# Kernel tuning notes

Measured on AMD Instinct MI355X. Metric: run time of the kernel, lower is better.

The kernel has to match this reference:

```python
import jax, jax.numpy as jnp
import numpy as np

LN_EPS = 1e-5


def setup_inputs() -> dict:
    key = jax.random.key(0)
    k1, k2 = jax.random.split(key, 2)
    B, C, D, H, W = 2, 96, 32, 128, 128
    out_dim = 2 * C
    x = jax.random.normal(k1, (B, C, D, H, W), dtype=jnp.float32)
    # nn.Linear(8*C, out_dim, bias=False): weight shape (out_dim, 8*C)
    w = jax.random.normal(k2, (out_dim, 8 * C), dtype=jnp.float32) * 0.02
    gamma = jnp.ones((8 * C,), dtype=jnp.float32)
    beta = jnp.zeros((8 * C,), dtype=jnp.float32)
    return {"x": x, "w": w, "gamma": gamma, "beta": beta}


def reference(x, w, gamma, beta):
    B, C, D, H, W = x.shape
    D2, H2, W2 = D // 2, H // 2, W // 2
    # Strided 2x2x2 gather: reshape then move (dd,hh,ww) offsets next to C.
    # torch.cat order [x0..x7] = (dd,hh,ww) lexicographic, dd most significant,
    # with C channels per block -> layout (..., dd, hh, ww, C) flattened.
    xr = x.reshape(B, C, D2, 2, H2, 2, W2, 2)
    xr = xr.transpose(0, 2, 4, 6, 3, 5, 7, 1)  # (B, D2, H2, W2, dd, hh, ww, C)
    xf = xr.reshape(B, D2, H2, W2, 8 * C)
    # LayerNorm over last dim
    mu = jnp.mean(xf, axis=-1, keepdims=True)
    xc = xf - mu
    var = jnp.mean(xc * xc, axis=-1, keepdims=True)
    xn = xc * jax.lax.rsqrt(var + LN_EPS) * gamma + beta
    # Linear (no bias): y = xn @ w.T
    y = jnp.einsum('bdhwc,oc->bdhwo', xn, w)
    # back to channels-first (B, out_dim, D2, H2, W2)
    return y.transpose(0, 4, 1, 2, 3)
```

## Files before the change

kernel.cpp:

```cpp
#include <hip/hip_runtime.h>
#include <hip/hip_bf16.h>

typedef __attribute__((ext_vector_type(8))) short short8;
typedef __attribute__((ext_vector_type(4))) float f32x4;

#define LN_EPS 1e-5f

__device__ __forceinline__ unsigned short f2bf(float f) {
  union { float f; unsigned u; } v; v.f = f;
  unsigned r = v.u + 0x7FFFu + ((v.u >> 16) & 1u);
  return (unsigned short)(r >> 16);
}

__device__ __forceinline__ int a_addr(int row, int colb) {
  return row * 1536 + (colb ^ ((row & 7) << 4));
}


__global__ __launch_bounds__(256) void pm_prep(
    const float* __restrict__ w, const float* __restrict__ g,
    const float* __restrict__ be, unsigned short* __restrict__ wg,
    float* __restrict__ sb) {
  const int o = blockIdx.x;
  const int t = threadIdx.x;
  __shared__ float red[256][2];
  float sa = 0.f, ba = 0.f;
#pragma unroll
  for (int u = 0; u < 3; ++u) {
    int kp = t + 256 * u;
    int dh = kp / 192;
    int rem = kp - dh * 192;
    int c = rem >> 1, ww = rem & 1;
    int k = dh * 192 + ww * 96 + c;
    float wv = w[o * 768 + k];
    float v = wv * g[k];
    sa += v;
    ba += wv * be[k];
    int NT = o >> 4, ks = kp >> 5, qq = (kp >> 3) & 3, jj = kp & 7;
    wg[(((NT * 24 + ks) * 64) + qq * 16 + (o & 15)) * 8 + jj] = f2bf(v);
  }
  red[t][0] = sa; red[t][1] = ba;
  __syncthreads();
  for (int s = 128; s > 0; s >>= 1) {
    if (t < s) { red[t][0] += red[t + s][0]; red[t][1] += red[t + s][1]; }
    __syncthreads();
  }
  if (t == 0) { sb[o] = red[0][0]; sb[192 + o] = red[0][1]; }
}

__global__ __launch_bounds__(256, 3) void pm_main(
    const float* __restrict__ x, const unsigned short* __restrict__ wg,
    const float* __restrict__ sb, float* __restrict__ out) {
  const int bid = blockIdx.x;
  const int wh = bid & 1;
  const int h2 = (bid >> 1) & 63;
  const int d2 = (bid >> 7) & 15;
  const int b = bid >> 11;
  const int t = threadIdx.x;
  const int lane = t & 63, wv = t >> 6;
  const int q = lane & 15, sc = lane >> 4;

  __shared__ __align__(16) unsigned char A_lds[32 * 1536];
  __shared__ float part[4][32][2];
  __shared__ float stats[32][2];

  const float* xb = x + (size_t)b * (96 * 32 * 128 * 128);
  const int cp0 = wv * 12 + sc * 3;
  const float* pc[3];
#pragma unroll
  for (int i = 0; i < 3; ++i)
    pc[i] = xb + (size_t)(2 * (cp0 + i)) * 524288 + wh * 64 + 4 * q;

  float sum0 = 0.f, sq0 = 0.f, sum1 = 0.f, sq1 = 0.f;
  float4 xa[3], xc[3];

  auto issue = [&](int p) {
    int off = (2 * d2 + (p >> 1)) * 16384 + (2 * h2 + (p & 1)) * 128;
#pragma unroll
    for (int i = 0; i < 3; ++i) {
      xa[i] = *(const float4*)(pc[i] + off);
      xc[i] = *(const float4*)(pc[i] + 524288 + off);
    }
  };

  auto consume = [&](int p) {
#pragma unroll
    for (int i = 0; i < 3; ++i) {
      float4 f0 = xa[i], f1 = xc[i];
      sum0 += (f0.x + f0.y) + (f1.x + f1.y);
      sq0  += f0.x * f0.x + f0.y * f0.y + f1.x * f1.x + f1.y * f1.y;
      sum1 += (f0.z + f0.w) + (f1.z + f1.w);
      sq1  += f0.z * f0.z + f0.w * f0.w + f1.z * f1.z + f1.w * f1.w;
      int colb = p * 384 + 8 * (cp0 + i);
      *(ushort4*)&A_lds[a_addr(2 * q, colb)] =
          make_ushort4(f2bf(f0.x), f2bf(f0.y), f2bf(f1.x), f2bf(f1.y));
      *(ushort4*)&A_lds[a_addr(2 * q + 1, colb)] =
          make_ushort4(f2bf(f0.z), f2bf(f0.w), f2bf(f1.z), f2bf(f1.w));
    }
  };

  const int al = lane & 15, ah = lane >> 4;
  const short8* wgs = (const short8*)wg;
  f32x4 acc[2][3];
#pragma unroll
  for (int mt = 0; mt < 2; ++mt)
#pragma unroll
    for (int nt = 0; nt < 3; ++nt) acc[mt][nt] = {0.f, 0.f, 0.f, 0.f};

  issue(0);

#pragma unroll
  for (int p = 0; p < 4; ++p) {
    consume(p);
    if (p == 3) {
      sum0 += __shfl_xor(sum0, 16); sum0 += __shfl_xor(sum0, 32);
      sq0  += __shfl_xor(sq0, 16);  sq0  += __shfl_xor(sq0, 32);
      sum1 += __shfl_xor(sum1, 16); sum1 += __shfl_xor(sum1, 32);
      sq1  += __shfl_xor(sq1, 16);  sq1  += __shfl_xor(sq1, 32);
      if (sc == 0) {
        part[wv][2 * q][0] = sum0;     part[wv][2 * q][1] = sq0;
        part[wv][2 * q + 1][0] = sum1; part[wv][2 * q + 1][1] = sq1;
      }
    }
    __syncthreads();

    short8 bfr[6][3];
#pragma unroll
    for (int ksi = 0; ksi < 6; ++ksi)
#pragma unroll
      for (int nt = 0; nt < 3; ++nt)
        bfr[ksi][nt] = wgs[((wv * 3 + nt) * 24 + (p * 6 + ksi)) * 64 + lane];

    if (p < 3) issue(p + 1);

    if (p == 3) {
      int row = t & 31;
      float S = part[0][row][0] + part[1][row][0] + part[2][row][0] + part[3][row][0];
      float Q = part[0][row][1] + part[1][row][1] + part[2][row][1] + part[3][row][1];
      float mu = S * (1.f / 768.f);
      float var = Q * (1.f / 768.f) - mu * mu;
      float rs = rsqrtf(var + LN_EPS);
      stats[row][0] = rs;
      stats[row][1] = mu * rs;
    }

#pragma unroll
    for (int ksi = 0; ksi < 6; ++ksi) {
      int ks = p * 6 + ksi;
      short8 afr[2];
#pragma unroll
      for (int mt = 0; mt < 2; ++mt)
        afr[mt] = *(const short8*)&A_lds[a_addr(mt * 16 + al, ks * 64 + ah * 16)];
#pragma unroll
      for (int nt = 0; nt < 3; ++nt)
#pragma unroll
        for (int mt = 0; mt < 2; ++mt)
          acc[mt][nt] = __builtin_amdgcn_mfma_f32_16x16x32_bf16(afr[mt], bfr[ksi][nt], acc[mt][nt], 0, 0, 0);
    }
  }
  __syncthreads();

#pragma unroll
  for (int nt = 0; nt < 3; ++nt) {
    int o = wv * 48 + nt * 16 + al;
    float Sv = sb[o], Bv = sb[192 + o];
    float* ob = out + (((size_t)(b * 192 + o) * 16 + d2) * 64 + h2) * 64 + wh * 32;
#pragma unroll
    for (int mt = 0; mt < 2; ++mt) {
      int m0 = mt * 16 + ah * 4;
      float4 y;
      y.x = stats[m0 + 0][0] * acc[mt][nt][0] - stats[m0 + 0][1] * Sv + Bv;
      y.y = stats[m0 + 1][0] * acc[mt][nt][1] - stats[m0 + 1][1] * Sv + Bv;
      y.z = stats[m0 + 2][0] * acc[mt][nt][2] - stats[m0 + 2][1] * Sv + Bv;
      y.w = stats[m0 + 3][0] * acc[mt][nt][3] - stats[m0 + 3][1] * Sv + Bv;
      *(float4*)(ob + m0) = y;
    }
  }
}

extern "C" void kernel_launch(void* const* d_in, const int* in_sizes, int n_in,
                              void* d_out, int out_size, void* d_ws, size_t ws_size,
                              hipStream_t stream) {
  (void)in_sizes; (void)n_in; (void)out_size; (void)ws_size;
  const float* x  = (const float*)d_in[0];
  const float* w  = (const float*)d_in[1];
  const float* g  = (const float*)d_in[2];
  const float* be = (const float*)d_in[3];
  unsigned short* wg = (unsigned short*)d_ws;
  float* sb = (float*)((char*)d_ws + 192 * 768 * sizeof(unsigned short));
  pm_prep<<<192, 256, 0, stream>>>(w, g, be, wg, sb);
  pm_main<<<4096, 256, 0, stream>>>(x, wg, sb, (float*)d_out);
}
```

Before: 149.9 us.

## Halve row tile per block to 16 rows and double grid for occupancy

Each block now processes 16 output positions instead of 32, with half the LDS staging buffer, one MFMA row tile, and a grid twice as large. Each thread loads a single float4 per channel and launch bounds request 4 blocks per CU. This aims to raise occupancy and memory-level parallelism for the x stream, at the cost of reloading the full bf16 weight fragments twice as often and less MFMA reuse per A fragment.

```diff
diff --git a/kernel.cpp b/kernel.cpp
--- a/kernel.cpp
+++ b/kernel.cpp
@@ -48,64 +48,55 @@
   if (t == 0) { sb[o] = red[0][0]; sb[192 + o] = red[0][1]; }
 }
 
-__global__ __launch_bounds__(256, 3) void pm_main(
+__global__ __launch_bounds__(256, 4) void pm_main(
     const float* __restrict__ x, const unsigned short* __restrict__ wg,
     const float* __restrict__ sb, float* __restrict__ out) {
   const int bid = blockIdx.x;
-  const int wh = bid & 1;
-  const int h2 = (bid >> 1) & 63;
-  const int d2 = (bid >> 7) & 15;
-  const int b = bid >> 11;
+  const int wq = bid & 3;
+  const int h2 = (bid >> 2) & 63;
+  const int d2 = (bid >> 8) & 15;
+  const int b = bid >> 12;
   const int t = threadIdx.x;
   const int lane = t & 63, wv = t >> 6;
-  const int q = lane & 15, sc = lane >> 4;
+  const int q = lane & 7, scc = lane >> 3;
 
-  __shared__ __align__(16) unsigned char A_lds[32 * 1536];
-  __shared__ float part[4][32][2];
-  __shared__ float stats[32][2];
+  __shared__ __align__(16) unsigned char A_lds[16 * 1536];
+  __shared__ float part[4][16][2];
+  __shared__ float stats[16][2];
 
   const float* xb = x + (size_t)b * (96 * 32 * 128 * 128);
-  const int cp0 = wv * 12 + sc * 3;
+  const int ct0 = wv * 24 + scc * 3;
   const float* pc[3];
 #pragma unroll
   for (int i = 0; i < 3; ++i)
-    pc[i] = xb + (size_t)(2 * (cp0 + i)) * 524288 + wh * 64 + 4 * q;
+    pc[i] = xb + (size_t)(ct0 + i) * 524288 + wq * 32 + 4 * q;
 
   float sum0 = 0.f, sq0 = 0.f, sum1 = 0.f, sq1 = 0.f;
-  float4 xa[3], xc[3];
+  float4 xa[3];
 
   auto issue = [&](int p) {
     int off = (2 * d2 + (p >> 1)) * 16384 + (2 * h2 + (p & 1)) * 128;
 #pragma unroll
-    for (int i = 0; i < 3; ++i) {
-      xa[i] = *(const float4*)(pc[i] + off);
-      xc[i] = *(const float4*)(pc[i] + 524288 + off);
-    }
+    for (int i = 0; i < 3; ++i) xa[i] = *(const float4*)(pc[i] + off);
   };
 
   auto consume = [&](int p) {
 #pragma unroll
     for (int i = 0; i < 3; ++i) {
-      float4 f0 = xa[i], f1 = xc[i];
-      sum0 += (f0.x + f0.y) + (f1.x + f1.y);
-      sq0  += f0.x * f0.x + f0.y * f0.y + f1.x * f1.x + f1.y * f1.y;
-      sum1 += (f0.z + f0.w) + (f1.z + f1.w);
-      sq1  += f0.z * f0.z + f0.w * f0.w + f1.z * f1.z + f1.w * f1.w;
-      int colb = p * 384 + 8 * (cp0 + i);
-      *(ushort4*)&A_lds[a_addr(2 * q, colb)] =
-          make_ushort4(f2bf(f0.x), f2bf(f0.y), f2bf(f1.x), f2bf(f1.y));
-      *(ushort4*)&A_lds[a_addr(2 * q + 1, colb)] =
-          make_ushort4(f2bf(f0.z), f2bf(f0.w), f2bf(f1.z), f2bf(f1.w));
+      float4 f = xa[i];
+      sum0 += f.x + f.y;  sq0 += f.x * f.x + f.y * f.y;
+      sum1 += f.z + f.w;  sq1 += f.z * f.z + f.w * f.w;
+      int colb = p * 384 + 4 * (ct0 + i);
+      *(ushort2*)&A_lds[a_addr(2 * q, colb)] = make_ushort2(f2bf(f.x), f2bf(f.y));
+      *(ushort2*)&A_lds[a_addr(2 * q + 1, colb)] = make_ushort2(f2bf(f.z), f2bf(f.w));
     }
   };
 
   const int al = lane & 15, ah = lane >> 4;
   const short8* wgs = (const short8*)wg;
-  f32x4 acc[2][3];
+  f32x4 acc[3];
 #pragma unroll
-  for (int mt = 0; mt < 2; ++mt)
-#pragma unroll
-    for (int nt = 0; nt < 3; ++nt) acc[mt][nt] = {0.f, 0.f, 0.f, 0.f};
+  for (int nt = 0; nt < 3; ++nt) acc[nt] = {0.f, 0.f, 0.f, 0.f};
 
   issue(0);
 
@@ -113,11 +104,11 @@
   for (int p = 0; p < 4; ++p) {
     consume(p);
     if (p == 3) {
-      sum0 += __shfl_xor(sum0, 16); sum0 += __shfl_xor(sum0, 32);
-      sq0  += __shfl_xor(sq0, 16);  sq0  += __shfl_xor(sq0, 32);
-      sum1 += __shfl_xor(sum1, 16); sum1 += __shfl_xor(sum1, 32);
-      sq1  += __shfl_xor(sq1, 16);  sq1  += __shfl_xor(sq1, 32);
-      if (sc == 0) {
+      sum0 += __shfl_xor(sum0, 8); sum0 += __shfl_xor(sum0, 16); sum0 += __shfl_xor(sum0, 32);
+      sq0  += __shfl_xor(sq0, 8);  sq0  += __shfl_xor(sq0, 16);  sq0  += __shfl_xor(sq0, 32);
+      sum1 += __shfl_xor(sum1, 8); sum1 += __shfl_xor(sum1, 16); sum1 += __shfl_xor(sum1, 32);
+      sq1  += __shfl_xor(sq1, 8);  sq1  += __shfl_xor(sq1, 16);  sq1  += __shfl_xor(sq1, 32);
+      if (scc == 0) {
         part[wv][2 * q][0] = sum0;     part[wv][2 * q][1] = sq0;
         part[wv][2 * q + 1][0] = sum1; part[wv][2 * q + 1][1] = sq1;
       }
@@ -134,7 +125,7 @@
     if (p < 3) issue(p + 1);
 
     if (p == 3) {
-      int row = t & 31;
+      int row = t & 15;
       float S = part[0][row][0] + part[1][row][0] + part[2][row][0] + part[3][row][0];
       float Q = part[0][row][1] + part[1][row][1] + part[2][row][1] + part[3][row][1];
       float mu = S * (1.f / 768.f);
@@ -147,15 +138,10 @@
 #pragma unroll
     for (int ksi = 0; ksi < 6; ++ksi) {
       int ks = p * 6 + ksi;
-      short8 afr[2];
-#pragma unroll
-      for (int mt = 0; mt < 2; ++mt)
-        afr[mt] = *(const short8*)&A_lds[a_addr(mt * 16 + al, ks * 64 + ah * 16)];
+      short8 afr = *(const short8*)&A_lds[a_addr(al, ks * 64 + ah * 16)];
 #pragma unroll
       for (int nt = 0; nt < 3; ++nt)
-#pragma unroll
-        for (int mt = 0; mt < 2; ++mt)
-          acc[mt][nt] = __builtin_amdgcn_mfma_f32_16x16x32_bf16(afr[mt], bfr[ksi][nt], acc[mt][nt], 0, 0, 0);
+        acc[nt] = __builtin_amdgcn_mfma_f32_16x16x32_bf16(afr, bfr[ksi][nt], acc[nt], 0, 0, 0);
     }
   }
   __syncthreads();
@@ -164,17 +150,14 @@
   for (int nt = 0; nt < 3; ++nt) {
     int o = wv * 48 + nt * 16 + al;
     float Sv = sb[o], Bv = sb[192 + o];
-    float* ob = out + (((size_t)(b * 192 + o) * 16 + d2) * 64 + h2) * 64 + wh * 32;
-#pragma unroll
-    for (int mt = 0; mt < 2; ++mt) {
-      int m0 = mt * 16 + ah * 4;
-      float4 y;
-      y.x = stats[m0 + 0][0] * acc[mt][nt][0] - stats[m0 + 0][1] * Sv + Bv;
-      y.y = stats[m0 + 1][0] * acc[mt][nt][1] - stats[m0 + 1][1] * Sv + Bv;
-      y.z = stats[m0 + 2][0] * acc[mt][nt][2] - stats[m0 + 2][1] * Sv + Bv;
-      y.w = stats[m0 + 3][0] * acc[mt][nt][3] - stats[m0 + 3][1] * Sv + Bv;
-      *(float4*)(ob + m0) = y;
-    }
+    float* ob = out + (((size_t)(b * 192 + o) * 16 + d2) * 64 + h2) * 64 + wq * 16;
+    int m0 = ah * 4;
+    float4 y;
+    y.x = stats[m0 + 0][0] * acc[nt][0] - stats[m0 + 0][1] * Sv + Bv;
+    y.y = stats[m0 + 1][0] * acc[nt][1] - stats[m0 + 1][1] * Sv + Bv;
+    y.z = stats[m0 + 2][0] * acc[nt][2] - stats[m0 + 2][1] * Sv + Bv;
+    y.w = stats[m0 + 3][0] * acc[nt][3] - stats[m0 + 3][1] * Sv + Bv;
+    *(float4*)(ob + m0) = y;
   }
 }
 
@@ -189,5 +172,5 @@
   unsigned short* wg = (unsigned short*)d_ws;
   float* sb = (float*)((char*)d_ws + 192 * 768 * sizeof(unsigned short));
   pm_prep<<<192, 256, 0, stream>>>(w, g, be, wg, sb);
-  pm_main<<<4096, 256, 0, stream>>>(x, wg, sb, (float*)d_out);
+  pm_main<<<8192, 256, 0, stream>>>(x, wg, sb, (float*)d_out);
 }
```

Result: slower. 208.0 us (+38.8%).
